# Optimization experiments

Measured on AMD Instinct MI355X. Metric: run time of the kernel, lower is better.

The kernel has to match this reference:

```python
import jax, jax.numpy as jnp
import numpy as np

N_NODES = 500_000
N_Q = 500_000
H = 8       # heads
MH = 8      # m // heads


def setup_inputs() -> dict:
    key = jax.random.key(0)
    ks = jax.random.split(key, 6)
    q_phi = jax.random.normal(ks[0], (N_Q, H, MH), dtype=jnp.float32)
    phi_k_pos = jax.random.normal(ks[1], (H, MH, N_NODES), dtype=jnp.float32)
    phi_k_neg = jax.random.normal(ks[2], (H, MH, N_NODES), dtype=jnp.float32)
    # degrees are nonnegative counts accumulated in build(); simulate with scaled uniforms
    deg_pos = jax.random.uniform(ks[3], (N_NODES, H), dtype=jnp.float32) * 32.0
    deg_neg = jax.random.uniform(ks[4], (N_NODES, H), dtype=jnp.float32) * 32.0
    k_indices = jax.random.randint(ks[5], (N_Q,), 0, N_NODES)
    return {
        "q_phi": q_phi,
        "phi_k_pos": phi_k_pos,
        "phi_k_neg": phi_k_neg,
        "deg_pos": deg_pos,
        "deg_neg": deg_neg,
        "k_indices": k_indices,
    }


def reference(q_phi, phi_k_pos, phi_k_neg, deg_pos, deg_neg, k_indices):
    # gather cached per-node random-feature sums: [h, mh, Nq] -> [Nq, h, mh]
    pk_pos = jnp.transpose(phi_k_pos[:, :, k_indices], (2, 0, 1))
    pk_neg = jnp.transpose(phi_k_neg[:, :, k_indices], (2, 0, 1))
    # per-head dot product over the feature chunk
    num_pos = jnp.sum(q_phi * pk_pos, axis=-1)  # [Nq, h]
    num_neg = jnp.sum(q_phi * pk_neg, axis=-1)  # [Nq, h]
    # degree-normalize with clamp_min(1)
    den_pos = jnp.maximum(deg_pos[k_indices], 1.0)  # [Nq, h]
    den_neg = jnp.maximum(deg_neg[k_indices], 1.0)
    return (num_pos / den_pos, num_neg / den_neg)
```

## Files before the change

kernel.cpp:

```cpp
#include <hip/hip_runtime.h>

constexpr int N_NODES = 500000;
constexpr int N_Q     = 500000;
constexpr int H       = 8;
constexpr int FEAT    = 64;

constexpr int TBIN   = 64;
constexpr int SHIFT  = 6;
constexpr int NB     = (N_NODES + TBIN - 1) / TBIN;
constexpr int NB_PAD = 8192;
constexpr int TP     = TBIN + 1;

__global__ __launch_bounds__(256) void zero_hist(int* __restrict__ hist)
{
    const int i = blockIdx.x * 256 + threadIdx.x;
    if (i < NB_PAD) hist[i] = 0;
}

__global__ __launch_bounds__(256) void hist_kernel(const int* __restrict__ k_idx,
                                                   int* __restrict__ hist)
{
    int i = blockIdx.x * blockDim.x + threadIdx.x;
    const int stride = gridDim.x * blockDim.x;
    for (; i < N_Q; i += stride)
        atomicAdd(&hist[k_idx[i] >> SHIFT], 1);
}

__global__ __launch_bounds__(1024) void scan_kernel(const int* __restrict__ hist,
                                                    int* __restrict__ offsets,
                                                    int* __restrict__ cursor)
{
    __shared__ int sums[1024];
    const int tid  = threadIdx.x;
    const int base = tid * 8;

    int loc[8];
    int run = 0;
#pragma unroll
    for (int k = 0; k < 8; ++k) {
        loc[k] = run;
        const int idx = base + k;
        run += (idx < NB) ? hist[idx] : 0;
    }
    sums[tid] = run;
    __syncthreads();

    const int own = run;
    for (int d = 1; d < 1024; d <<= 1) {
        const int add = (tid >= d) ? sums[tid - d] : 0;
        __syncthreads();
        sums[tid] += add;
        __syncthreads();
    }
    const int excl = sums[tid] - own;

#pragma unroll
    for (int k = 0; k < 8; ++k) {
        const int idx = base + k;
        if (idx <= NB) {
            const int v = excl + loc[k];
            offsets[idx] = v;
            cursor[idx]  = v;
        }
    }
}

__global__ __launch_bounds__(256) void scatter_kernel(const int* __restrict__ k_idx,
                                                      int* __restrict__ cursor,
                                                      unsigned* __restrict__ vals)
{
    int i = blockIdx.x * blockDim.x + threadIdx.x;
    const int stride = gridDim.x * blockDim.x;
    for (; i < N_Q; i += stride) {
        const int j = k_idx[i];
        const int b = j >> SHIFT;
        const int p = atomicAdd(&cursor[b], 1);
        vals[p] = ((unsigned)i << SHIFT) | (unsigned)(j & (TBIN - 1));
    }
}

__global__ __launch_bounds__(256, 4) void iskde_binned(
    const float* __restrict__ q_phi,
    const float* __restrict__ pk_pos,
    const float* __restrict__ pk_neg,
    const float* __restrict__ deg_pos,
    const float* __restrict__ deg_neg,
    const unsigned* __restrict__ vals,
    const int* __restrict__ offsets,
    float* __restrict__ out)
{
    __shared__ float lds[2][FEAT][TP];

    const int tid  = threadIdx.x;
    const int b    = blockIdx.x;
    const int n0   = b * TBIN;
    const int nrem = min(TBIN, N_NODES - n0);

#pragma unroll
    for (int s = 0; s < 2; ++s) {
        const float* __restrict__ src = s ? pk_neg : pk_pos;
#pragma unroll
        for (int it = 0; it < 4; ++it) {
            const int g  = it * 256 + tid;
            const int f  = g >> 4;
            const int n4 = (g & 15) * 4;
            const float* p = src + (size_t)f * N_NODES + n0 + n4;
            float4 v = make_float4(0.f, 0.f, 0.f, 0.f);
            if (n4 + 3 < nrem) {
                v = *(const float4*)p;
            } else {
                if (n4 + 0 < nrem) v.x = p[0];
                if (n4 + 1 < nrem) v.y = p[1];
                if (n4 + 2 < nrem) v.z = p[2];
                if (n4 + 3 < nrem) v.w = p[3];
            }
            float* l = &lds[s][f][n4];
            l[0] = v.x; l[1] = v.y; l[2] = v.z; l[3] = v.w;
        }
    }
    __syncthreads();

    const int start = offsets[b];
    const int count = offsets[b + 1] - start;
    const int h    = tid & 7;
    const int slot = tid >> 3;

    for (int it0 = 0; it0 < count; it0 += 32) {
        const int qi    = it0 + slot;
        const bool valid = qi < count;
        unsigned v = 0;
        if (valid) v = vals[start + qi];
        const int q  = (int)(v >> SHIFT);
        const int dj = (int)(v & (TBIN - 1));

        const float4* qp = (const float4*)(q_phi + (size_t)q * FEAT + h * 8);
        const float4 a0 = qp[0];
        const float4 a1 = qp[1];

        const float* lp = &lds[0][h * 8][dj];
        const float* ln = &lds[1][h * 8][dj];
        float sp = a0.x * lp[0]      + a0.y * lp[TP]     + a0.z * lp[2 * TP] + a0.w * lp[3 * TP]
                 + a1.x * lp[4 * TP] + a1.y * lp[5 * TP] + a1.z * lp[6 * TP] + a1.w * lp[7 * TP];
        float sn = a0.x * ln[0]      + a0.y * ln[TP]     + a0.z * ln[2 * TP] + a0.w * ln[3 * TP]
                 + a1.x * ln[4 * TP] + a1.y * ln[5 * TP] + a1.z * ln[6 * TP] + a1.w * ln[7 * TP];

        const int j = n0 + dj;
        const float dp = fmaxf(deg_pos[(size_t)j * H + h], 1.0f);
        const float dn = fmaxf(deg_neg[(size_t)j * H + h], 1.0f);

        if (valid) {
            const size_t o = (size_t)q * H + h;
            __builtin_nontemporal_store(sp / dp, &out[o]);
            __builtin_nontemporal_store(sn / dn, &out[(size_t)N_Q * H + o]);
        }
    }
}

__global__ __launch_bounds__(256, 4) void iskde_gather_kernel(
    const float* __restrict__ q_phi,
    const float* __restrict__ pk_pos,
    const float* __restrict__ pk_neg,
    const float* __restrict__ deg_pos,
    const float* __restrict__ deg_neg,
    const int*   __restrict__ k_idx,
    float*       __restrict__ out)
{
    const int wave_in_blk = threadIdx.x >> 6;
    const int lane        = threadIdx.x & 63;
    const int q           = blockIdx.x * 4 + wave_in_blk;
    if (q >= N_Q) return;

    const int j = k_idx[q];
    const float qv = q_phi[(size_t)q * FEAT + lane];
    const size_t col = (size_t)lane * (size_t)N_NODES + (size_t)j;
    const float pv = pk_pos[col];
    const float nv = pk_neg[col];

    float sp = qv * pv;
    float sn = qv * nv;
    sp += __shfl_xor(sp, 1, 64);
    sn += __shfl_xor(sn, 1, 64);
    sp += __shfl_xor(sp, 2, 64);
    sn += __shfl_xor(sn, 2, 64);
    sp += __shfl_xor(sp, 4, 64);
    sn += __shfl_xor(sn, 4, 64);

    if ((lane & 7) == 0) {
        const int h = lane >> 3;
        const float dp = fmaxf(deg_pos[(size_t)j * H + h], 1.0f);
        const float dn = fmaxf(deg_neg[(size_t)j * H + h], 1.0f);
        const size_t o = (size_t)q * H + h;
        out[o]                   = sp / dp;
        out[(size_t)N_Q * H + o] = sn / dn;
    }
}

extern "C" void kernel_launch(void* const* d_in, const int* in_sizes, int n_in,
                              void* d_out, int out_size, void* d_ws, size_t ws_size,
                              hipStream_t stream) {
    const float* q_phi   = (const float*)d_in[0];
    const float* pk_pos  = (const float*)d_in[1];
    const float* pk_neg  = (const float*)d_in[2];
    const float* deg_pos = (const float*)d_in[3];
    const float* deg_neg = (const float*)d_in[4];
    const int*   k_idx   = (const int*)d_in[5];
    float*       out     = (float*)d_out;

    const size_t need = ((size_t)NB_PAD * 3 + 16 + (size_t)N_Q) * sizeof(int);

    if (ws_size >= need) {
        int*      hist    = (int*)d_ws;
        int*      offsets = hist + NB_PAD;
        int*      cursor  = offsets + NB_PAD + 8;
        unsigned* vals    = (unsigned*)(cursor + NB_PAD + 8);

        zero_hist<<<(NB_PAD + 255) / 256, 256, 0, stream>>>(hist);
        hist_kernel<<<1024, 256, 0, stream>>>(k_idx, hist);
        scan_kernel<<<1, 1024, 0, stream>>>(hist, offsets, cursor);
        scatter_kernel<<<1024, 256, 0, stream>>>(k_idx, cursor, vals);
        iskde_binned<<<NB, 256, 0, stream>>>(
            q_phi, pk_pos, pk_neg, deg_pos, deg_neg, vals, offsets, out);
    } else {
        const int blocks = (N_Q + 3) / 4;
        iskde_gather_kernel<<<blocks, 256, 0, stream>>>(
            q_phi, pk_pos, pk_neg, deg_pos, deg_neg, k_idx, out);
    }
}
```

Measured before the change: 469.7 us.

## Widen binned block to 512 threads and overlap first query loads with tile staging

The binned kernel now runs 512 threads per block, so 64 query slots cover a bin's roughly 64 queries in one pass. The first round's query index, q_phi and degree loads are issued before the shared-memory tile barrier, so their latency overlaps the tile staging. The histogram and scatter kernels switch from grid-stride loops over 1024 blocks to one thread per query. The wider block may limit occupancy and adds register pressure from the hoisted loads.

```diff
diff --git a/kernel.cpp b/kernel.cpp
--- a/kernel.cpp
+++ b/kernel.cpp
@@ -10,6 +10,8 @@
 constexpr int NB     = (N_NODES + TBIN - 1) / TBIN;
 constexpr int NB_PAD = 8192;
 constexpr int TP     = TBIN + 1;
+constexpr int BT     = 512;
+constexpr int SLOTS  = BT / H;
 
 __global__ __launch_bounds__(256) void zero_hist(int* __restrict__ hist)
 {
@@ -20,10 +22,8 @@
 __global__ __launch_bounds__(256) void hist_kernel(const int* __restrict__ k_idx,
                                                    int* __restrict__ hist)
 {
-    int i = blockIdx.x * blockDim.x + threadIdx.x;
-    const int stride = gridDim.x * blockDim.x;
-    for (; i < N_Q; i += stride)
-        atomicAdd(&hist[k_idx[i] >> SHIFT], 1);
+    const int i = blockIdx.x * 256 + threadIdx.x;
+    if (i < N_Q) atomicAdd(&hist[k_idx[i] >> SHIFT], 1);
 }
 
 __global__ __launch_bounds__(1024) void scan_kernel(const int* __restrict__ hist,
@@ -69,9 +69,8 @@
                                                       int* __restrict__ cursor,
                                                       unsigned* __restrict__ vals)
 {
-    int i = blockIdx.x * blockDim.x + threadIdx.x;
-    const int stride = gridDim.x * blockDim.x;
-    for (; i < N_Q; i += stride) {
+    const int i = blockIdx.x * 256 + threadIdx.x;
+    if (i < N_Q) {
         const int j = k_idx[i];
         const int b = j >> SHIFT;
         const int p = atomicAdd(&cursor[b], 1);
@@ -79,7 +78,7 @@
     }
 }
 
-__global__ __launch_bounds__(256, 4) void iskde_binned(
+__global__ __launch_bounds__(BT, 8) void iskde_binned(
     const float* __restrict__ q_phi,
     const float* __restrict__ pk_pos,
     const float* __restrict__ pk_neg,
@@ -96,37 +95,62 @@
     const int n0   = b * TBIN;
     const int nrem = min(TBIN, N_NODES - n0);
 
-#pragma unroll
-    for (int s = 0; s < 2; ++s) {
-        const float* __restrict__ src = s ? pk_neg : pk_pos;
-#pragma unroll
-        for (int it = 0; it < 4; ++it) {
-            const int g  = it * 256 + tid;
-            const int f  = g >> 4;
-            const int n4 = (g & 15) * 4;
-            const float* p = src + (size_t)f * N_NODES + n0 + n4;
-            float4 v = make_float4(0.f, 0.f, 0.f, 0.f);
-            if (n4 + 3 < nrem) {
-                v = *(const float4*)p;
-            } else {
-                if (n4 + 0 < nrem) v.x = p[0];
-                if (n4 + 1 < nrem) v.y = p[1];
-                if (n4 + 2 < nrem) v.z = p[2];
-                if (n4 + 3 < nrem) v.w = p[3];
-            }
-            float* l = &lds[s][f][n4];
-            l[0] = v.x; l[1] = v.y; l[2] = v.z; l[3] = v.w;
-        }
-    }
-    __syncthreads();
-
     const int start = offsets[b];
     const int count = offsets[b + 1] - start;
     const int h    = tid & 7;
     const int slot = tid >> 3;
 
-    for (int it0 = 0; it0 < count; it0 += 32) {
-        const int qi    = it0 + slot;
+    const bool v0ok = slot < count;
+    unsigned v0 = 0;
+    if (v0ok) v0 = vals[start + slot];
+
+#pragma unroll
+    for (int it = 0; it < 4; ++it) {
+        const int g  = it * BT + tid;
+        const int s  = g >> 10;
+        const int f  = (g >> 4) & 63;
+        const int n4 = (g & 15) * 4;
+        const float* __restrict__ src = s ? pk_neg : pk_pos;
+        const float* p = src + (size_t)f * N_NODES + n0 + n4;
+        float4 w = make_float4(0.f, 0.f, 0.f, 0.f);
+        if (n4 + 3 < nrem) {
+            w = *(const float4*)p;
+        } else {
+            if (n4 + 0 < nrem) w.x = p[0];
+            if (n4 + 1 < nrem) w.y = p[1];
+            if (n4 + 2 < nrem) w.z = p[2];
+        }
+        float* l = &lds[s][f][n4];
+        l[0] = w.x; l[1] = w.y; l[2] = w.z; l[3] = w.w;
+    }
+
+    const int q0  = (int)(v0 >> SHIFT);
+    const int dj0 = (int)(v0 & (TBIN - 1));
+    const float4* qp0 = (const float4*)(q_phi + (size_t)q0 * FEAT + h * 8);
+    const float4 a0 = qp0[0];
+    const float4 a1 = qp0[1];
+    const int   j0   = n0 + dj0;
+    const float dgp0 = deg_pos[(size_t)j0 * H + h];
+    const float dgn0 = deg_neg[(size_t)j0 * H + h];
+
+    __syncthreads();
+
+    if (v0ok) {
+        const float* lp = &lds[0][h * 8][dj0];
+        const float* ln = &lds[1][h * 8][dj0];
+        float sp = a0.x * lp[0]      + a0.y * lp[TP]     + a0.z * lp[2 * TP] + a0.w * lp[3 * TP]
+                 + a1.x * lp[4 * TP] + a1.y * lp[5 * TP] + a1.z * lp[6 * TP] + a1.w * lp[7 * TP];
+        float sn = a0.x * ln[0]      + a0.y * ln[TP]     + a0.z * ln[2 * TP] + a0.w * ln[3 * TP]
+                 + a1.x * ln[4 * TP] + a1.y * ln[5 * TP] + a1.z * ln[6 * TP] + a1.w * ln[7 * TP];
+        const float dp = fmaxf(dgp0, 1.0f);
+        const float dn = fmaxf(dgn0, 1.0f);
+        const size_t o = (size_t)q0 * H + h;
+        __builtin_nontemporal_store(sp / dp, &out[o]);
+        __builtin_nontemporal_store(sn / dn, &out[(size_t)N_Q * H + o]);
+    }
+
+    for (int it0 = SLOTS; it0 < count; it0 += SLOTS) {
+        const int qi     = it0 + slot;
         const bool valid = qi < count;
         unsigned v = 0;
         if (valid) v = vals[start + qi];
@@ -134,15 +158,15 @@
         const int dj = (int)(v & (TBIN - 1));
 
         const float4* qp = (const float4*)(q_phi + (size_t)q * FEAT + h * 8);
-        const float4 a0 = qp[0];
-        const float4 a1 = qp[1];
+        const float4 b0 = qp[0];
+        const float4 b1 = qp[1];
 
         const float* lp = &lds[0][h * 8][dj];
         const float* ln = &lds[1][h * 8][dj];
-        float sp = a0.x * lp[0]      + a0.y * lp[TP]     + a0.z * lp[2 * TP] + a0.w * lp[3 * TP]
-                 + a1.x * lp[4 * TP] + a1.y * lp[5 * TP] + a1.z * lp[6 * TP] + a1.w * lp[7 * TP];
-        float sn = a0.x * ln[0]      + a0.y * ln[TP]     + a0.z * ln[2 * TP] + a0.w * ln[3 * TP]
-                 + a1.x * ln[4 * TP] + a1.y * ln[5 * TP] + a1.z * ln[6 * TP] + a1.w * ln[7 * TP];
+        float sp = b0.x * lp[0]      + b0.y * lp[TP]     + b0.z * lp[2 * TP] + b0.w * lp[3 * TP]
+                 + b1.x * lp[4 * TP] + b1.y * lp[5 * TP] + b1.z * lp[6 * TP] + b1.w * lp[7 * TP];
+        float sn = b0.x * ln[0]      + b0.y * ln[TP]     + b0.z * ln[2 * TP] + b0.w * ln[3 * TP]
+                 + b1.x * ln[4 * TP] + b1.y * ln[5 * TP] + b1.z * ln[6 * TP] + b1.w * ln[7 * TP];
 
         const int j = n0 + dj;
         const float dp = fmaxf(deg_pos[(size_t)j * H + h], 1.0f);
@@ -214,11 +238,12 @@
         int*      cursor  = offsets + NB_PAD + 8;
         unsigned* vals    = (unsigned*)(cursor + NB_PAD + 8);
 
+        const int qblocks = (N_Q + 255) / 256;
         zero_hist<<<(NB_PAD + 255) / 256, 256, 0, stream>>>(hist);
-        hist_kernel<<<1024, 256, 0, stream>>>(k_idx, hist);
+        hist_kernel<<<qblocks, 256, 0, stream>>>(k_idx, hist);
         scan_kernel<<<1, 1024, 0, stream>>>(hist, offsets, cursor);
-        scatter_kernel<<<1024, 256, 0, stream>>>(k_idx, cursor, vals);
-        iskde_binned<<<NB, 256, 0, stream>>>(
+        scatter_kernel<<<qblocks, 256, 0, stream>>>(k_idx, cursor, vals);
+        iskde_binned<<<NB, BT, 0, stream>>>(
             q_phi, pk_pos, pk_neg, deg_pos, deg_neg, vals, offsets, out);
     } else {
         const int blocks = (N_Q + 3) / 4;
```

Measured after the change: 439.7 us. -6.4%, faster.

## Use chunked LDS histograms for binning and pipeline multi-bin blocks in main kernel

Applied to the files above, without the earlier changes.

The binning pre-pass replaces global-atomic histogram and scatter with per-chunk shared-memory histograms, a column sum, a scan and per-chunk base offsets, so atomics hit LDS instead of global memory. The main kernel now processes four bins per 512-thread block. It prefetches the next bin's feature tile, first query and degrees into registers while computing the current bin, which overlaps global loads with compute. The cost is extra small kernels, a larger workspace, only 64 blocks in the scatter phase, and a stage_load that zero-fills any partial float4 tail instead of loading it element by element.

```diff
diff --git a/kernel.cpp b/kernel.cpp
--- a/kernel.cpp
+++ b/kernel.cpp
@@ -10,25 +10,43 @@
 constexpr int NB     = (N_NODES + TBIN - 1) / TBIN;
 constexpr int NB_PAD = 8192;
 constexpr int TP     = TBIN + 1;
-
-__global__ __launch_bounds__(256) void zero_hist(int* __restrict__ hist)
-{
-    const int i = blockIdx.x * 256 + threadIdx.x;
-    if (i < NB_PAD) hist[i] = 0;
-}
-
-__global__ __launch_bounds__(256) void hist_kernel(const int* __restrict__ k_idx,
-                                                   int* __restrict__ hist)
-{
-    int i = blockIdx.x * blockDim.x + threadIdx.x;
-    const int stride = gridDim.x * blockDim.x;
-    for (; i < N_Q; i += stride)
-        atomicAdd(&hist[k_idx[i] >> SHIFT], 1);
-}
-
-__global__ __launch_bounds__(1024) void scan_kernel(const int* __restrict__ hist,
-                                                    int* __restrict__ offsets,
-                                                    int* __restrict__ cursor)
+constexpr int BT     = 512;
+constexpr int SLOTS  = BT / H;
+constexpr int KBINS  = 4;
+constexpr int NCHUNK = 64;
+constexpr int CHUNK  = (N_Q + NCHUNK - 1) / NCHUNK;
+
+__global__ __launch_bounds__(1024) void hist_chunks(const int* __restrict__ k_idx,
+                                                    int* __restrict__ hist)
+{
+    __shared__ int lh[NB];
+    const int c = blockIdx.x, tid = threadIdx.x;
+    for (int i = tid; i < NB; i += 1024) lh[i] = 0;
+    __syncthreads();
+    const int i0 = c * CHUNK;
+    const int i1 = min(i0 + CHUNK, N_Q);
+    for (int i = i0 + tid; i < i1; i += 1024)
+        atomicAdd(&lh[k_idx[i] >> SHIFT], 1);
+    __syncthreads();
+    int* hrow = hist + (size_t)c * NB;
+    for (int i = tid; i < NB; i += 1024) hrow[i] = lh[i];
+}
+
+__global__ __launch_bounds__(256) void tot_kernel(const int* __restrict__ hist,
+                                                  int* __restrict__ tot)
+{
+    const int b = blockIdx.x * 256 + threadIdx.x;
+    if (b < NB) {
+        int s = 0;
+        for (int c = 0; c < NCHUNK; ++c) s += hist[(size_t)c * NB + b];
+        tot[b] = s;
+    } else if (b < NB_PAD) {
+        tot[b] = 0;
+    }
+}
+
+__global__ __launch_bounds__(1024) void scan_kernel(const int* __restrict__ tot,
+                                                    int* __restrict__ offsets)
 {
     __shared__ int sums[1024];
     const int tid  = threadIdx.x;
@@ -40,7 +58,7 @@
     for (int k = 0; k < 8; ++k) {
         loc[k] = run;
         const int idx = base + k;
-        run += (idx < NB) ? hist[idx] : 0;
+        run += (idx < NB) ? tot[idx] : 0;
     }
     sums[tid] = run;
     __syncthreads();
@@ -57,29 +75,76 @@
 #pragma unroll
     for (int k = 0; k < 8; ++k) {
         const int idx = base + k;
-        if (idx <= NB) {
-            const int v = excl + loc[k];
-            offsets[idx] = v;
-            cursor[idx]  = v;
-        }
-    }
-}
-
-__global__ __launch_bounds__(256) void scatter_kernel(const int* __restrict__ k_idx,
-                                                      int* __restrict__ cursor,
-                                                      unsigned* __restrict__ vals)
-{
-    int i = blockIdx.x * blockDim.x + threadIdx.x;
-    const int stride = gridDim.x * blockDim.x;
-    for (; i < N_Q; i += stride) {
+        if (idx <= NB) offsets[idx] = excl + loc[k];
+    }
+}
+
+__global__ __launch_bounds__(256) void base_kernel(const int* __restrict__ hist,
+                                                   const int* __restrict__ offsets,
+                                                   int* __restrict__ base)
+{
+    const int b = blockIdx.x * 256 + threadIdx.x;
+    if (b < NB) {
+        int run = offsets[b];
+        for (int c = 0; c < NCHUNK; ++c) {
+            base[(size_t)c * NB + b] = run;
+            run += hist[(size_t)c * NB + b];
+        }
+    }
+}
+
+__global__ __launch_bounds__(1024) void scatter_chunks(const int* __restrict__ k_idx,
+                                                       const int* __restrict__ base,
+                                                       unsigned* __restrict__ vals)
+{
+    __shared__ int cur[NB];
+    const int c = blockIdx.x, tid = threadIdx.x;
+    const int* brow = base + (size_t)c * NB;
+    for (int i = tid; i < NB; i += 1024) cur[i] = brow[i];
+    __syncthreads();
+    const int i0 = c * CHUNK;
+    const int i1 = min(i0 + CHUNK, N_Q);
+    for (int i = i0 + tid; i < i1; i += 1024) {
         const int j = k_idx[i];
         const int b = j >> SHIFT;
-        const int p = atomicAdd(&cursor[b], 1);
+        const int p = atomicAdd(&cur[b], 1);
         vals[p] = ((unsigned)i << SHIFT) | (unsigned)(j & (TBIN - 1));
     }
 }
 
-__global__ __launch_bounds__(256, 4) void iskde_binned(
+__device__ __forceinline__ void stage_load(const float* __restrict__ pk_pos,
+                                           const float* __restrict__ pk_neg,
+                                           int f0, int n4, int n0, int nrem,
+                                           float4 r[4])
+{
+    const float* p0 = pk_pos + (size_t)f0 * N_NODES + n0 + n4;
+    const float* p1 = pk_pos + (size_t)(f0 + 32) * N_NODES + n0 + n4;
+    const float* p2 = pk_neg + (size_t)f0 * N_NODES + n0 + n4;
+    const float* p3 = pk_neg + (size_t)(f0 + 32) * N_NODES + n0 + n4;
+    if (n4 + 3 < nrem) {
+        r[0] = *(const float4*)p0;
+        r[1] = *(const float4*)p1;
+        r[2] = *(const float4*)p2;
+        r[3] = *(const float4*)p3;
+    } else {
+        r[0] = r[1] = r[2] = r[3] = make_float4(0.f, 0.f, 0.f, 0.f);
+    }
+}
+
+__device__ __forceinline__ void stage_write(float (*lds)[FEAT][TP],
+                                            int f0, int n4, const float4 r[4])
+{
+    float* l0 = &lds[0][f0][n4];
+    float* l1 = &lds[0][f0 + 32][n4];
+    float* l2 = &lds[1][f0][n4];
+    float* l3 = &lds[1][f0 + 32][n4];
+    l0[0] = r[0].x; l0[1] = r[0].y; l0[2] = r[0].z; l0[3] = r[0].w;
+    l1[0] = r[1].x; l1[1] = r[1].y; l1[2] = r[1].z; l1[3] = r[1].w;
+    l2[0] = r[2].x; l2[1] = r[2].y; l2[2] = r[2].z; l2[3] = r[2].w;
+    l3[0] = r[3].x; l3[1] = r[3].y; l3[2] = r[3].z; l3[3] = r[3].w;
+}
+
+__global__ __launch_bounds__(BT, 8) void iskde_binned(
     const float* __restrict__ q_phi,
     const float* __restrict__ pk_pos,
     const float* __restrict__ pk_neg,
@@ -92,67 +157,106 @@
     __shared__ float lds[2][FEAT][TP];
 
     const int tid  = threadIdx.x;
-    const int b    = blockIdx.x;
-    const int n0   = b * TBIN;
-    const int nrem = min(TBIN, N_NODES - n0);
-
-#pragma unroll
-    for (int s = 0; s < 2; ++s) {
-        const float* __restrict__ src = s ? pk_neg : pk_pos;
-#pragma unroll
-        for (int it = 0; it < 4; ++it) {
-            const int g  = it * 256 + tid;
-            const int f  = g >> 4;
-            const int n4 = (g & 15) * 4;
-            const float* p = src + (size_t)f * N_NODES + n0 + n4;
-            float4 v = make_float4(0.f, 0.f, 0.f, 0.f);
-            if (n4 + 3 < nrem) {
-                v = *(const float4*)p;
-            } else {
-                if (n4 + 0 < nrem) v.x = p[0];
-                if (n4 + 1 < nrem) v.y = p[1];
-                if (n4 + 2 < nrem) v.z = p[2];
-                if (n4 + 3 < nrem) v.w = p[3];
-            }
-            float* l = &lds[s][f][n4];
-            l[0] = v.x; l[1] = v.y; l[2] = v.z; l[3] = v.w;
-        }
-    }
-    __syncthreads();
-
-    const int start = offsets[b];
-    const int count = offsets[b + 1] - start;
     const int h    = tid & 7;
     const int slot = tid >> 3;
-
-    for (int it0 = 0; it0 < count; it0 += 32) {
-        const int qi    = it0 + slot;
-        const bool valid = qi < count;
-        unsigned v = 0;
-        if (valid) v = vals[start + qi];
-        const int q  = (int)(v >> SHIFT);
-        const int dj = (int)(v & (TBIN - 1));
-
-        const float4* qp = (const float4*)(q_phi + (size_t)q * FEAT + h * 8);
-        const float4 a0 = qp[0];
-        const float4 a1 = qp[1];
-
-        const float* lp = &lds[0][h * 8][dj];
-        const float* ln = &lds[1][h * 8][dj];
-        float sp = a0.x * lp[0]      + a0.y * lp[TP]     + a0.z * lp[2 * TP] + a0.w * lp[3 * TP]
-                 + a1.x * lp[4 * TP] + a1.y * lp[5 * TP] + a1.z * lp[6 * TP] + a1.w * lp[7 * TP];
-        float sn = a0.x * ln[0]      + a0.y * ln[TP]     + a0.z * ln[2 * TP] + a0.w * ln[3 * TP]
-                 + a1.x * ln[4 * TP] + a1.y * ln[5 * TP] + a1.z * ln[6 * TP] + a1.w * ln[7 * TP];
-
-        const int j = n0 + dj;
-        const float dp = fmaxf(deg_pos[(size_t)j * H + h], 1.0f);
-        const float dn = fmaxf(deg_neg[(size_t)j * H + h], 1.0f);
-
-        if (valid) {
+    const int f0   = tid >> 4;
+    const int n4   = (tid & 15) * 4;
+
+    const int b0 = blockIdx.x * KBINS;
+    const int nb = min(KBINS, NB - b0);
+
+    float4 r[4];
+    {
+        const int n0   = b0 * TBIN;
+        const int nrem = min(TBIN, N_NODES - n0);
+        stage_load(pk_pos, pk_neg, f0, n4, n0, nrem, r);
+    }
+
+    int off0 = offsets[b0];
+    int off1 = offsets[b0 + 1];
+    int cnt  = off1 - off0;
+    unsigned v = (slot < cnt) ? vals[off0 + slot] : 0u;
+    int q  = (int)(v >> SHIFT);
+    int dj = (int)(v & (TBIN - 1));
+    const float4* qp = (const float4*)(q_phi + (size_t)q * FEAT + h * 8);
+    float4 a0 = qp[0];
+    float4 a1 = qp[1];
+    float dgp = deg_pos[(size_t)(b0 * TBIN + dj) * H + h];
+    float dgn = deg_neg[(size_t)(b0 * TBIN + dj) * H + h];
+
+    for (int i = 0; i < nb; ++i) {
+        const int b  = b0 + i;
+        const int n0 = b * TBIN;
+
+        stage_write(lds, f0, n4, r);
+
+        if (i + 1 < nb) {
+            const int n0n   = (b + 1) * TBIN;
+            const int nremn = min(TBIN, N_NODES - n0n);
+            stage_load(pk_pos, pk_neg, f0, n4, n0n, nremn, r);
+        }
+
+        int off0n = 0, cntn = 0;
+        unsigned vn = 0u;
+        if (i + 1 < nb) {
+            off0n = off1;
+            const int off1n = offsets[min(b + 2, NB)];
+            cntn = off1n - off0n;
+            if (slot < cntn) vn = vals[off0n + slot];
+            off1 = off1n;
+        }
+        __syncthreads();
+
+        if (slot < cnt) {
+            const float* lp = &lds[0][h * 8][dj];
+            const float* ln = &lds[1][h * 8][dj];
+            float sp = a0.x*lp[0]      + a0.y*lp[TP]     + a0.z*lp[2*TP] + a0.w*lp[3*TP]
+                     + a1.x*lp[4*TP]   + a1.y*lp[5*TP]   + a1.z*lp[6*TP] + a1.w*lp[7*TP];
+            float sn = a0.x*ln[0]      + a0.y*ln[TP]     + a0.z*ln[2*TP] + a0.w*ln[3*TP]
+                     + a1.x*ln[4*TP]   + a1.y*ln[5*TP]   + a1.z*ln[6*TP] + a1.w*ln[7*TP];
+            const float dp = fmaxf(dgp, 1.0f);
+            const float dn = fmaxf(dgn, 1.0f);
             const size_t o = (size_t)q * H + h;
             __builtin_nontemporal_store(sp / dp, &out[o]);
             __builtin_nontemporal_store(sn / dn, &out[(size_t)N_Q * H + o]);
         }
+
+        for (int it0 = SLOTS; it0 < cnt; it0 += SLOTS) {
+            const int qi  = it0 + slot;
+            const bool ok = qi < cnt;
+            const unsigned vt = ok ? vals[off0 + qi] : 0u;
+            const int qt  = (int)(vt >> SHIFT);
+            const int djt = (int)(vt & (TBIN - 1));
+            const float4* qpt = (const float4*)(q_phi + (size_t)qt * FEAT + h * 8);
+            const float4 c0 = qpt[0];
+            const float4 c1 = qpt[1];
+            const float* lp = &lds[0][h * 8][djt];
+            const float* ln = &lds[1][h * 8][djt];
+            float sp = c0.x*lp[0]      + c0.y*lp[TP]     + c0.z*lp[2*TP] + c0.w*lp[3*TP]
+                     + c1.x*lp[4*TP]   + c1.y*lp[5*TP]   + c1.z*lp[6*TP] + c1.w*lp[7*TP];
+            float sn = c0.x*ln[0]      + c0.y*ln[TP]     + c0.z*ln[2*TP] + c0.w*ln[3*TP]
+                     + c1.x*ln[4*TP]   + c1.y*ln[5*TP]   + c1.z*ln[6*TP] + c1.w*ln[7*TP];
+            const float dp = fmaxf(deg_pos[(size_t)(n0 + djt) * H + h], 1.0f);
+            const float dn = fmaxf(deg_neg[(size_t)(n0 + djt) * H + h], 1.0f);
+            if (ok) {
+                const size_t o = (size_t)qt * H + h;
+                __builtin_nontemporal_store(sp / dp, &out[o]);
+                __builtin_nontemporal_store(sn / dn, &out[(size_t)N_Q * H + o]);
+            }
+        }
+
+        if (i + 1 < nb) {
+            q  = (int)(vn >> SHIFT);
+            dj = (int)(vn & (TBIN - 1));
+            const float4* qpn = (const float4*)(q_phi + (size_t)q * FEAT + h * 8);
+            a0 = qpn[0];
+            a1 = qpn[1];
+            dgp = deg_pos[(size_t)((b + 1) * TBIN + dj) * H + h];
+            dgn = deg_neg[(size_t)((b + 1) * TBIN + dj) * H + h];
+            off0 = off0n;
+            cnt  = cntn;
+        }
+        __syncthreads();
     }
 }
 
@@ -206,19 +310,24 @@
     const int*   k_idx   = (const int*)d_in[5];
     float*       out     = (float*)d_out;
 
-    const size_t need = ((size_t)NB_PAD * 3 + 16 + (size_t)N_Q) * sizeof(int);
+    const size_t CN   = (size_t)NCHUNK * NB;
+    const size_t need = (2 * CN + NB_PAD + NB_PAD + 8 + (size_t)N_Q) * sizeof(int);
 
     if (ws_size >= need) {
         int*      hist    = (int*)d_ws;
-        int*      offsets = hist + NB_PAD;
-        int*      cursor  = offsets + NB_PAD + 8;
-        unsigned* vals    = (unsigned*)(cursor + NB_PAD + 8);
-
-        zero_hist<<<(NB_PAD + 255) / 256, 256, 0, stream>>>(hist);
-        hist_kernel<<<1024, 256, 0, stream>>>(k_idx, hist);
-        scan_kernel<<<1, 1024, 0, stream>>>(hist, offsets, cursor);
-        scatter_kernel<<<1024, 256, 0, stream>>>(k_idx, cursor, vals);
-        iskde_binned<<<NB, 256, 0, stream>>>(
+        int*      base    = hist + CN;
+        int*      tot     = base + CN;
+        int*      offsets = tot + NB_PAD;
+        unsigned* vals    = (unsigned*)(offsets + NB_PAD + 8);
+
+        hist_chunks<<<NCHUNK, 1024, 0, stream>>>(k_idx, hist);
+        tot_kernel<<<NB_PAD / 256, 256, 0, stream>>>(hist, tot);
+        scan_kernel<<<1, 1024, 0, stream>>>(tot, offsets);
+        base_kernel<<<NB_PAD / 256, 256, 0, stream>>>(hist, offsets, base);
+        scatter_chunks<<<NCHUNK, 1024, 0, stream>>>(k_idx, base, vals);
+
+        const int mgrid = (NB + KBINS - 1) / KBINS;
+        iskde_binned<<<mgrid, BT, 0, stream>>>(
             q_phi, pk_pos, pk_neg, deg_pos, deg_neg, vals, offsets, out);
     } else {
         const int blocks = (N_Q + 3) / 4;
```

Result: no change. 462.2 us (-1.6%).
